# Kernel tuning notes

Measured on AMD Instinct MI355X. Metric: run time of the kernel, lower is better.

## Reference

```python
import jax, jax.numpy as jnp
import numpy as np


def setup_inputs() -> dict:
    key = jax.random.key(0)
    z = jax.random.normal(key, (8, 4096, 1024), dtype=jnp.float32)
    return {"z": z}


def reference(z):
    d = z.shape[-1]
    # sort descending along last dim
    z_sorted = -jnp.sort(-z, axis=-1)
    z_cumsum = jnp.cumsum(z_sorted, axis=-1)
    k = jnp.arange(1, d + 1, dtype=z.dtype)  # [d]
    rhs = 1 + k * z_sorted
    is_gt = (rhs > z_cumsum).astype(z.dtype)
    # largest k satisfying the support condition
    k_z = jnp.max(is_gt * k, axis=-1, keepdims=True)  # [..., 1]
    idx = k_z.astype(jnp.int32) - 1
    z_cumsum_k = jnp.take_along_axis(z_cumsum, idx, axis=-1)
    tau = (z_cumsum_k - 1) / k_z
    p = jnp.clip(z - tau, 0.0, None)
    return p
```

## Files before the change

### kernel.cpp

```cpp
#include <hip/hip_runtime.h>


#define ROW_D 1024

typedef float f4 __attribute__((ext_vector_type(4)));

template <int CTRL, int RMASK>
__device__ __forceinline__ float dpp_mv(float x) {
    return __builtin_bit_cast(float, __builtin_amdgcn_update_dpp(
        __builtin_bit_cast(int, x), __builtin_bit_cast(int, x),
        CTRL, RMASK, 0xf, false));
}

__device__ __forceinline__ float dpp_sum_to63(float x) {
    x += dpp_mv<0x111, 0xf>(x);
    x += dpp_mv<0x112, 0xf>(x);
    x += dpp_mv<0x114, 0xf>(x);
    x += dpp_mv<0x118, 0xf>(x);
    x += dpp_mv<0x142, 0xa>(x);
    x += dpp_mv<0x143, 0xc>(x);
    return x;
}
__device__ __forceinline__ float dpp_max_to63(float x) {
    x = fmaxf(x, dpp_mv<0x111, 0xf>(x));
    x = fmaxf(x, dpp_mv<0x112, 0xf>(x));
    x = fmaxf(x, dpp_mv<0x114, 0xf>(x));
    x = fmaxf(x, dpp_mv<0x118, 0xf>(x));
    x = fmaxf(x, dpp_mv<0x142, 0xa>(x));
    x = fmaxf(x, dpp_mv<0x143, 0xc>(x));
    return x;
}
__device__ __forceinline__ float bcast63(float x) {
    return __builtin_bit_cast(float,
        __builtin_amdgcn_readlane(__builtin_bit_cast(int, x), 63));
}
__device__ __forceinline__ float fast_rcp(float x) {
    float r;
    asm("v_rcp_f32 %0, %1" : "=v"(r) : "v"(x));
    return r;
}

__device__ __forceinline__ void ce(float& a, float& b) {
    const float hi = fmaxf(a, b);
    const float lo = fminf(a, b);
    a = hi; b = lo;
}
__device__ __forceinline__ void sort4(float& a, float& b, float& c, float& d) {
    ce(a, b); ce(c, d); ce(a, c); ce(b, d); ce(b, c);
}
__device__ __forceinline__ void merge44_top4(
    float A0, float A1, float A2, float A3,
    float B0, float B1, float B2, float B3,
    float& R0, float& R1, float& R2, float& R3) {
    float e0 = A0, e1 = A2, e2 = B0, e3 = B2;
    ce(e0, e2); ce(e1, e3); ce(e1, e2);
    float o0 = A1, o1 = A3, o2 = B1, o3 = B3;
    ce(o0, o2); ce(o1, o3); ce(o1, o2);
    R0 = e0;
    float x = o0, y = e1;
    ce(x, y);
    R1 = x; R2 = y;
    R3 = fmaxf(o1, e2);
}

__device__ __forceinline__ void prefetch_row(const float* __restrict__ z,
                                             int row, int lane,
                                             float* ldsbase) {
    const char* g = (const char*)(z + (size_t)row * ROW_D) + (size_t)lane * 16;
#pragma unroll
    for (int j = 0; j < 4; ++j) {
        __builtin_amdgcn_global_load_lds(
            (const __attribute__((address_space(1))) void*)(g + j * 1024),
            (__attribute__((address_space(3))) void*)(ldsbase + j * 256),
            16, 0, 0);
    }
}

__device__ __forceinline__ float solve_tau(const f4 (&v)[4]) {
    float g[4][4];
#pragma unroll
    for (int j = 0; j < 4; ++j) {
        g[j][0] = v[j].x; g[j][1] = v[j].y; g[j][2] = v[j].z; g[j][3] = v[j].w;
        sort4(g[j][0], g[j][1], g[j][2], g[j][3]);
    }
    float a0, a1, a2, a3, b0, b1, b2, b3, T0, T1, T2, T3;
    merge44_top4(g[0][0], g[0][1], g[0][2], g[0][3],
                 g[1][0], g[1][1], g[1][2], g[1][3], a0, a1, a2, a3);
    merge44_top4(g[2][0], g[2][1], g[2][2], g[2][3],
                 g[3][0], g[3][1], g[3][2], g[3][3], b0, b1, b2, b3);
    merge44_top4(a0, a1, a2, a3, b0, b1, b2, b3, T0, T1, T2, T3);

    const float m = bcast63(dpp_max_to63(T0));
    float t = m - 1.0f;

    if (__ballot(T3 > t) == 0ull) {
#pragma unroll 1
        for (int it = 0; it < 16; ++it) {
            const float d0 = T0 - t, d1 = T1 - t, d2 = T2 - t, d3 = T3 - t;
            const float Sl = (fmaxf(d0, 0.0f) + fmaxf(d1, 0.0f)) +
                             (fmaxf(d2, 0.0f) + fmaxf(d3, 0.0f));
            int n = __popcll(__ballot(d0 > 0.0f));
            n += __popcll(__ballot(d1 > 0.0f));
            n += __popcll(__ballot(d2 > 0.0f));
            n += __popcll(__ballot(d3 > 0.0f));
            const float S = bcast63(dpp_sum_to63(Sl));
            const float step = (S - 1.0f) * fast_rcp((float)n);
            t += step;
            if (step <= 1e-6f) break;
        }
    } else {
#pragma unroll 1
        for (int it = 0; it < 16; ++it) {
            float sj[4];
            int n = 0;
#pragma unroll
            for (int j = 0; j < 4; ++j) {
                const float d0 = v[j].x - t, d1 = v[j].y - t;
                const float d2 = v[j].z - t, d3 = v[j].w - t;
                sj[j] = (fmaxf(d0, 0.0f) + fmaxf(d1, 0.0f)) +
                        (fmaxf(d2, 0.0f) + fmaxf(d3, 0.0f));
                n += __popcll(__ballot(d0 > 0.0f));
                n += __popcll(__ballot(d1 > 0.0f));
                n += __popcll(__ballot(d2 > 0.0f));
                n += __popcll(__ballot(d3 > 0.0f));
            }
            const float S = bcast63(dpp_sum_to63((sj[0] + sj[1]) + (sj[2] + sj[3])));
            const float step = (S - 1.0f) * fast_rcp((float)n);
            t += step;
            if (step <= 1e-6f) break;
        }
    }
    return t;
}

__device__ __forceinline__ void store_row(const f4 (&v)[4], float t,
                                          float* __restrict__ out,
                                          int row, int lane) {
    f4* __restrict__ p = reinterpret_cast<f4*>(out + (size_t)row * ROW_D);
#pragma unroll
    for (int j = 0; j < 4; ++j) {
        f4 o;
        o.x = fmaxf(v[j].x - t, 0.0f);
        o.y = fmaxf(v[j].y - t, 0.0f);
        o.z = fmaxf(v[j].z - t, 0.0f);
        o.w = fmaxf(v[j].w - t, 0.0f);
        p[lane + 64 * j] = o;
    }
}

__global__ __launch_bounds__(256) void sparsemax_kernel(
    const float* __restrict__ z, float* __restrict__ out, int nrows) {
    const int lane = (int)(threadIdx.x & 63u);
    const int w    = (int)(threadIdx.x >> 6);
    int r = (int)(blockIdx.x << 2) + w;
    const int W = (int)(gridDim.x << 2);
    if (r >= nrows) return;

    __shared__ float lds[4][2][ROW_D];

    f4 v[4];
    {
        const f4* __restrict__ zin = reinterpret_cast<const f4*>(z + (size_t)r * ROW_D);
#pragma unroll
        for (int j = 0; j < 4; ++j) v[j] = zin[lane + 64 * j];
    }
    int rn = r + W;
    int s = 0;
    if (rn < nrows) prefetch_row(z, rn, lane, &lds[w][0][0]);
    __builtin_amdgcn_sched_barrier(0);

    for (;;) {
        const float t = solve_tau(v);
        const int rf = rn + W;
        if (rn < nrows && rf < nrows)
            prefetch_row(z, rf, lane, &lds[w][s ^ 1][0]);
        __builtin_amdgcn_sched_barrier(0);
        store_row(v, t, out, r, lane);
        if (rn >= nrows) break;

        asm volatile("s_waitcnt vmcnt(8)" ::: "memory");
        __builtin_amdgcn_sched_barrier(0);
        const f4* lsrc = reinterpret_cast<const f4*>(&lds[w][s][0]);
#pragma unroll
        for (int j = 0; j < 4; ++j) v[j] = lsrc[lane + 64 * j];

        r = rn; rn = rf; s ^= 1;
    }
}

extern "C" void kernel_launch(void* const* d_in, const int* in_sizes, int n_in,
                              void* d_out, int out_size, void* d_ws, size_t ws_size,
                              hipStream_t stream) {
    const float* z = (const float*)d_in[0];
    float* out = (float*)d_out;
    const int n = in_sizes[0];
    const int nrows = n / ROW_D;
    int blocks = 512;
    const int max_blocks = (nrows + 3) >> 2;
    if (blocks > max_blocks) blocks = max_blocks;
    sparsemax_kernel<<<blocks, 256, 0, stream>>>(z, out, nrows);
}
```

Measured before the change: 229.9 us.

## Deepen per-wave row pipeline to triple-buffered LDS prefetch with more blocks

Replaces the double-buffered loop with a three-slot LDS ring per wave that keeps three rows of global_load_lds prefetch in flight, using explicit vmcnt waits tuned to outstanding loads and stores. The grid grows from 512 to 768 blocks, and small inputs fall back to a simple one-row-per-wave kernel. The aim is to hide more memory latency and raise achieved bandwidth. In exchange it uses more LDS per block and hand-counted waitcnts that are fragile if instruction counts change.

```diff
diff --git a/kernel.cpp b/kernel.cpp
--- a/kernel.cpp
+++ b/kernel.cpp
@@ -148,44 +148,85 @@
     }
 }
 
-__global__ __launch_bounds__(256) void sparsemax_kernel(
+__device__ __forceinline__ void pipe_step(const float* __restrict__ z,
+                                          float* __restrict__ out,
+                                          float* slot, int k, int kdma,
+                                          int lane, bool do_dma) {
+    f4 v[4];
+    const f4* lsrc = reinterpret_cast<const f4*>(slot);
+#pragma unroll
+    for (int j = 0; j < 4; ++j) v[j] = lsrc[lane + 64 * j];
+    const float t = solve_tau(v);
+    __builtin_amdgcn_sched_barrier(0);
+    if (do_dma) prefetch_row(z, kdma, lane, slot);
+    __builtin_amdgcn_sched_barrier(0);
+    store_row(v, t, out, k, lane);
+    __builtin_amdgcn_sched_barrier(0);
+}
+
+#define WAIT_VM(N) do { \
+    asm volatile("s_waitcnt vmcnt(" #N ")" ::: "memory"); \
+    __builtin_amdgcn_sched_barrier(0); } while (0)
+
+__global__ __launch_bounds__(256) void sparsemax_pipe(
     const float* __restrict__ z, float* __restrict__ out, int nrows) {
     const int lane = (int)(threadIdx.x & 63u);
     const int w    = (int)(threadIdx.x >> 6);
-    int r = (int)(blockIdx.x << 2) + w;
-    const int W = (int)(gridDim.x << 2);
-    if (r >= nrows) return;
-
-    __shared__ float lds[4][2][ROW_D];
-
+    const int wid  = (int)(blockIdx.x << 2) + w;
+    const int W    = (int)(gridDim.x << 2);
+    if (wid >= nrows) return;
+
+    __shared__ float lds[4][3][ROW_D];
+    float* slot0 = &lds[w][0][0];
+    float* slot1 = &lds[w][1][0];
+    float* slot2 = &lds[w][2][0];
+
+    const int T = (nrows - wid + W - 1) / W;
+
+    int k = wid;
+    prefetch_row(z, k,         lane, slot0);
+    prefetch_row(z, k + W,     lane, slot1);
+    prefetch_row(z, k + 2 * W, lane, slot2);
+    __builtin_amdgcn_sched_barrier(0);
+
+    WAIT_VM(8);
+    pipe_step(z, out, slot0, k, k + 3 * W, lane, true); k += W;
+    WAIT_VM(12);
+    pipe_step(z, out, slot1, k, k + 3 * W, lane, true); k += W;
+    WAIT_VM(16);
+    pipe_step(z, out, slot2, k, k + 3 * W, lane, true); k += W;
+
+    float* slots[3] = {slot0, slot1, slot2};
+    int s = 0;
+#pragma unroll 1
+    for (int i = 3; i + 3 < T; ++i) {
+        WAIT_VM(20);
+        pipe_step(z, out, slots[s], k, k + 3 * W, lane, true);
+        k += W;
+        s = (s == 2) ? 0 : s + 1;
+    }
+
+    WAIT_VM(20);
+    pipe_step(z, out, slots[s], k, 0, lane, false); k += W;
+    s = (s == 2) ? 0 : s + 1;
+    WAIT_VM(16);
+    pipe_step(z, out, slots[s], k, 0, lane, false); k += W;
+    s = (s == 2) ? 0 : s + 1;
+    WAIT_VM(12);
+    pipe_step(z, out, slots[s], k, 0, lane, false);
+}
+
+__global__ __launch_bounds__(256) void sparsemax_simple(
+    const float* __restrict__ z, float* __restrict__ out, int nrows) {
+    const int lane = (int)(threadIdx.x & 63u);
+    const int row  = (int)(blockIdx.x << 2) + (int)(threadIdx.x >> 6);
+    if (row >= nrows) return;
+    const f4* __restrict__ zin = reinterpret_cast<const f4*>(z + (size_t)row * ROW_D);
     f4 v[4];
-    {
-        const f4* __restrict__ zin = reinterpret_cast<const f4*>(z + (size_t)r * ROW_D);
-#pragma unroll
-        for (int j = 0; j < 4; ++j) v[j] = zin[lane + 64 * j];
-    }
-    int rn = r + W;
-    int s = 0;
-    if (rn < nrows) prefetch_row(z, rn, lane, &lds[w][0][0]);
-    __builtin_amdgcn_sched_barrier(0);
-
-    for (;;) {
-        const float t = solve_tau(v);
-        const int rf = rn + W;
-        if (rn < nrows && rf < nrows)
-            prefetch_row(z, rf, lane, &lds[w][s ^ 1][0]);
-        __builtin_amdgcn_sched_barrier(0);
-        store_row(v, t, out, r, lane);
-        if (rn >= nrows) break;
-
-        asm volatile("s_waitcnt vmcnt(8)" ::: "memory");
-        __builtin_amdgcn_sched_barrier(0);
-        const f4* lsrc = reinterpret_cast<const f4*>(&lds[w][s][0]);
-#pragma unroll
-        for (int j = 0; j < 4; ++j) v[j] = lsrc[lane + 64 * j];
-
-        r = rn; rn = rf; s ^= 1;
-    }
+#pragma unroll
+    for (int j = 0; j < 4; ++j) v[j] = zin[lane + 64 * j];
+    const float t = solve_tau(v);
+    store_row(v, t, out, row, lane);
 }
 
 extern "C" void kernel_launch(void* const* d_in, const int* in_sizes, int n_in,
@@ -195,8 +236,12 @@
     float* out = (float*)d_out;
     const int n = in_sizes[0];
     const int nrows = n / ROW_D;
-    int blocks = 512;
-    const int max_blocks = (nrows + 3) >> 2;
-    if (blocks > max_blocks) blocks = max_blocks;
-    sparsemax_kernel<<<blocks, 256, 0, stream>>>(z, out, nrows);
-}
+
+    const int blocks = 768;
+    const int W = blocks * 4;
+    if (nrows >= 6 * W) {
+        sparsemax_pipe<<<blocks, 256, 0, stream>>>(z, out, nrows);
+    } else {
+        sparsemax_simple<<<(nrows + 3) / 4, 256, 0, stream>>>(z, out, nrows);
+    }
+}
```

Result: no change. 233.6 us (+1.6%).
